# Performance work log

Measured on AMD Instinct MI355X. Metric: run time of the kernel, lower is better.

## Reference

```python
import jax, jax.numpy as jnp
import numpy as np

B, S, H = 2, 2048, 1024
NH, DH = 16, 64  # num heads, head dim

def setup_inputs() -> dict:
    key = jax.random.key(0)
    ks = jax.random.split(key, 4)
    scale = 0.02
    return {
        "hidden_states": jax.random.normal(ks[0], (B, S, H), dtype=jnp.float32),
        "attention_mask": jnp.zeros((B, 1, 1, S), dtype=jnp.float32),  # additive mask
        "Wq": jax.random.normal(ks[1], (H, H), dtype=jnp.float32) * scale,
        "bq": jnp.zeros((H,), dtype=jnp.float32),
        "Wk": jax.random.normal(ks[2], (H, H), dtype=jnp.float32) * scale,
        "bk": jnp.zeros((H,), dtype=jnp.float32),
        "Wv": jax.random.normal(ks[3], (H, H), dtype=jnp.float32) * scale,
        "bv": jnp.zeros((H,), dtype=jnp.float32),
    }

def _split_heads(x):
    # [B,S,H] -> [B,NH,S,DH]
    return x.reshape(B, S, NH, DH).transpose(0, 2, 1, 3)

def reference(hidden_states, attention_mask, Wq, bq, Wk, bk, Wv, bv):
    q = _split_heads(hidden_states @ Wq + bq)
    k = _split_heads(hidden_states @ Wk + bk)
    v = _split_heads(hidden_states @ Wv + bv)
    # scores: [B,NH,S,S]
    scores = jnp.einsum('bhqd,bhkd->bhqk', q, k) / jnp.asarray(np.sqrt(DH), scores_dtype := q.dtype)
    scores = scores + attention_mask  # additive mask broadcast
    probs = jax.nn.softmax(scores, axis=-1)
    out = jnp.einsum('bhqk,bhkd->bhqd', probs, v)  # [B,NH,S,DH]
    out = out.transpose(0, 2, 1, 3).reshape(B, S, H)
    return out
```

## Files before the change

kernel.cpp:

```cpp
#include <hip/hip_runtime.h>
#include <hip/hip_bf16.h>

#define Bn  2
#define Sn  2048
#define Hn  1024
#define NHn 16
#define DHn 64
#define Mn  (Bn * Sn)

typedef __attribute__((ext_vector_type(4)))  float    f32x4;
typedef __attribute__((ext_vector_type(16))) float    f32x16;
typedef __attribute__((ext_vector_type(8)))  _Float16 h8;
typedef __attribute__((ext_vector_type(4)))  _Float16 h4;
typedef __attribute__((ext_vector_type(2)))  __fp16   fp16x2;
typedef __attribute__((ext_vector_type(2)))  unsigned int u32x2;

union H2PK { fp16x2 v; unsigned int u; };
union U4H8 { unsigned int u[4]; h8 v; };

#define MFMA16F(a, b, c) __builtin_amdgcn_mfma_f32_16x16x32_f16(a, b, c, 0, 0, 0)
#define MFMA32F(a, b, c) __builtin_amdgcn_mfma_f32_32x32x16_f16(a, b, c, 0, 0, 0)

#define SCFULL 0.18033688011112042f
#define L2E    1.44269504088896340736f

__device__ __forceinline__ void glds16(const void* g, void* l) {
    __builtin_amdgcn_global_load_lds(
        (const __attribute__((address_space(1))) unsigned int*)g,
        (__attribute__((address_space(3))) unsigned int*)l, 16, 0, 0);
}

__global__ __launch_bounds__(256) void prep(
    const float* __restrict__ X, const float* __restrict__ W0,
    const float* __restrict__ W1, const float* __restrict__ W2,
    _Float16* __restrict__ Xh, _Float16* __restrict__ WT)
{
    const int bid = blockIdx.x;
    const int tid = threadIdx.x;
    __shared__ float Ws[64][65];

    if (bid < 4096) {
        const int i = bid * 256 + tid;
        float4 x = ((const float4*)X)[i];
        h4 o;
        o[0] = (_Float16)x.x; o[1] = (_Float16)x.y;
        o[2] = (_Float16)x.z; o[3] = (_Float16)x.w;
        *(h4*)&Xh[(size_t)i * 4] = o;
        return;
    }

    const int wb = bid - 4096;
    const int which = wb >> 8;
    const int rem = wb & 255;
    const int k0 = ((rem >> 4) & 15) * 64;
    const int n0 = (rem & 15) * 64;
    const float* W = (which == 0) ? W0 : (which == 1 ? W1 : W2);
    _Float16* O = WT + (size_t)which * Hn * Hn;

#pragma unroll
    for (int it = 0; it < 4; ++it) {
        const int idx = tid + 256 * it;
        const int row = idx >> 4, c4 = (idx & 15) * 4;
        float4 w = *(const float4*)&W[(size_t)(k0 + row) * Hn + n0 + c4];
        Ws[row][c4 + 0] = w.x; Ws[row][c4 + 1] = w.y;
        Ws[row][c4 + 2] = w.z; Ws[row][c4 + 3] = w.w;
    }
    __syncthreads();
#pragma unroll
    for (int it = 0; it < 16; ++it) {
        const int e = tid + 256 * it;
        const int k = e & 63, n = e >> 6;
        O[(size_t)(n0 + n) * Hn + k0 + k] = (_Float16)Ws[k][n];
    }
}

__global__ __launch_bounds__(256) void qkv_mfma(
    const _Float16* __restrict__ Xh, const _Float16* __restrict__ WTA,
    const float* __restrict__ b0, const float* __restrict__ b1,
    const float* __restrict__ b2,
    _Float16* __restrict__ Qh, _Float16* __restrict__ Kh,
    _Float16* __restrict__ VTh)
{
    const int which = blockIdx.z;
    const _Float16* WT = WTA + (size_t)which * Hn * Hn;
    const float* bias = (which == 0) ? b0 : (which == 1 ? b1 : b2);
    _Float16* Dst = (which == 0) ? Qh : (which == 1 ? Kh : VTh);

    const int m0 = blockIdx.x * 128;
    const int n0 = blockIdx.y * 128;
    const int tid  = threadIdx.x;
    const int wid  = tid >> 6;
    const int lane = tid & 63;
    const int l16  = lane & 15;
    const int quad = lane >> 4;
    const int wm = wid >> 1, wn = wid & 1;

    __shared__ _Float16 Ah[128 * 64], Bh[128 * 64];

    f32x4 acc[4][4];
#pragma unroll
    for (int i = 0; i < 4; ++i)
#pragma unroll
        for (int j = 0; j < 4; ++j) acc[i][j] = (f32x4){0.f, 0.f, 0.f, 0.f};

    for (int kt = 0; kt < Hn / 64; ++kt) {
        const int k0 = kt * 64;
        __syncthreads();
#pragma unroll
        for (int c = 0; c < 4; ++c) {
            const int idx = (wid * 4 + c) * 64 + lane;
            const int row = idx >> 3;
            const int cg  = (idx & 7) ^ (row & 7);
            glds16(&Xh[(size_t)(m0 + row) * Hn + k0 + cg * 8],
                   &Ah[(wid * 4 + c) * 512]);
            glds16(&WT[(size_t)(n0 + row) * Hn + k0 + cg * 8],
                   &Bh[(wid * 4 + c) * 512]);
        }
        __syncthreads();

#pragma unroll
        for (int kk = 0; kk < 2; ++kk) {
            h8 xa[4], wb[4];
#pragma unroll
            for (int t = 0; t < 4; ++t) {
                const int ar = wm * 64 + t * 16 + l16;
                const int br = wn * 64 + t * 16 + l16;
                xa[t] = *(const h8*)&Ah[ar * 64 + (((kk * 4 + quad) ^ (ar & 7)) * 8)];
                wb[t] = *(const h8*)&Bh[br * 64 + (((kk * 4 + quad) ^ (br & 7)) * 8)];
            }
            if (which < 2) {
#pragma unroll
                for (int i = 0; i < 4; ++i)
#pragma unroll
                    for (int j = 0; j < 4; ++j)
                        acc[i][j] = MFMA16F(xa[i], wb[j], acc[i][j]);
            } else {
#pragma unroll
                for (int i = 0; i < 4; ++i)
#pragma unroll
                    for (int j = 0; j < 4; ++j)
                        acc[i][j] = MFMA16F(wb[i], xa[j], acc[i][j]);
            }
        }
    }

    const float oscale = (which == 0) ? SCFULL : 1.0f;
    if (which < 2) {
#pragma unroll
        for (int j = 0; j < 4; ++j) {
            const int n = n0 + wn * 64 + j * 16 + l16;
            const float bv = bias[n];
            const int hh = n >> 6, dd = n & 63;
#pragma unroll
            for (int i = 0; i < 4; ++i) {
                const int mb = m0 + wm * 64 + i * 16 + quad * 4;
#pragma unroll
                for (int r = 0; r < 4; ++r) {
                    const int m = mb + r;
                    const int b = m >> 11, s = m & (Sn - 1);
                    Dst[(((size_t)b * NHn + hh) * Sn + s) * DHn + dd] =
                        (_Float16)((acc[i][j][r] + bv) * oscale);
                }
            }
        }
    } else {
#pragma unroll
        for (int i = 0; i < 4; ++i) {
#pragma unroll
            for (int r = 0; r < 4; ++r) {
                const int n = n0 + wn * 64 + i * 16 + quad * 4 + r;
                const float bv = bias[n];
                const int hh = n >> 6, dd = n & 63;
#pragma unroll
                for (int j = 0; j < 4; ++j) {
                    const int m = m0 + wm * 64 + j * 16 + l16;
                    const int b = m >> 11, s = m & (Sn - 1);
                    Dst[(((size_t)b * NHn + hh) * DHn + dd) * Sn + s] =
                        (_Float16)(acc[i][j][r] + bv);
                }
            }
        }
    }
}

__global__ __launch_bounds__(256, 2) void attn(
    const _Float16* __restrict__ Qh, const _Float16* __restrict__ Kh,
    const _Float16* __restrict__ VTh, const float* __restrict__ mask,
    float* __restrict__ Out)
{
    const int flat = blockIdx.x + 16 * blockIdx.y + 256 * blockIdx.z;
    const int bh   = ((flat & 7) << 2) | ((flat >> 3) & 3);
    const int qb   = flat >> 5;
    const int b = bh >> 4, h = bh & 15;

    const int tid  = threadIdx.x;
    const int wid  = tid >> 6;
    const int lane = tid & 63;
    const int l32  = lane & 31;
    const int hi   = lane >> 5;

    __shared__ __align__(16) _Float16 Kb[4][4096];
    __shared__ __align__(16) _Float16 Vb[4][4096];
    __shared__ float4 Ml4[Sn / 4];
    const float* Ml = (const float*)Ml4;

    const int q0 = qb * 128 + wid * 32;

    const float4* mg = (const float4*)(mask + (size_t)b * Sn);
    float4 m0v = mg[tid], m1v = mg[tid + 256];

    const size_t qbase = ((size_t)bh * Sn + q0 + l32) * DHn;
    h8 qf[4];
#pragma unroll
    for (int kd = 0; kd < 4; ++kd)
        qf[kd] = *(const h8*)&Qh[qbase + kd * 16 + hi * 8];

    asm volatile("s_waitcnt vmcnt(0)" ::: "memory");

    {
        float4 a0 = {m0v.x * L2E, m0v.y * L2E, m0v.z * L2E, m0v.w * L2E};
        float4 a1 = {m1v.x * L2E, m1v.y * L2E, m1v.z * L2E, m1v.w * L2E};
        Ml4[tid] = a0;
        Ml4[tid + 256] = a1;
    }

    const _Float16* Kg = Kh  + (size_t)bh * Sn * DHn;
    const _Float16* Vg = VTh + (size_t)bh * DHn * Sn;

    auto stage = [&](int kt, int buf) {
        const int koff = kt * 64;
#pragma unroll
        for (int c = 0; c < 2; ++c) {
            const int idx = (wid * 2 + c) * 64 + lane;
            const int row = idx >> 3;
            const int cg  = (idx & 7) ^ (row & 7);
            glds16(&Kg[(size_t)(koff + row) * DHn + cg * 8],
                   &Kb[buf][(wid * 2 + c) * 512]);
            glds16(&Vg[(size_t)row * Sn + koff + cg * 8],
                   &Vb[buf][(wid * 2 + c) * 512]);
        }
    };

    stage(0, 0);
    stage(1, 1);

    f32x16 sA[2], sB[2], o[2], acc_l;
#pragma unroll
    for (int dt = 0; dt < 2; ++dt) o[dt] = (f32x16)(0.f);
    acc_l = (f32x16)(0.f);

    h8 ones;
#pragma unroll
    for (int j = 0; j < 8; ++j) ones[j] = (_Float16)1.0f;

    auto qkt = [&](f32x16 (&s)[2], int buf, int ktile) {
        __builtin_amdgcn_s_setprio(1);
#pragma unroll
        for (int t = 0; t < 2; ++t) {
            f32x16 c;
#pragma unroll
            for (int g = 0; g < 4; ++g) {
                float4 mv = *(const float4*)&Ml[ktile * 64 + t * 32 + hi * 4 + g * 8];
                c[g * 4 + 0] = mv.x; c[g * 4 + 1] = mv.y;
                c[g * 4 + 2] = mv.z; c[g * 4 + 3] = mv.w;
            }
#pragma unroll
            for (int kd = 0; kd < 4; ++kd) {
                const int row = t * 32 + l32;
                h8 kf = *(const h8*)&Kb[buf][row * 64 +
                                             (((kd * 2 + hi) ^ (row & 7)) * 8)];
                c = MFMA32F(kf, qf[kd], c);
            }
            s[t] = c;
        }
        __builtin_amdgcn_s_setprio(0);
    };

    auto sm_pv = [&](f32x16 (&s)[2], int buf) {
        unsigned int pk[2][4][2];
#pragma unroll
        for (int t = 0; t < 2; ++t) {
#pragma unroll
            for (int g = 0; g < 4; ++g) {
                const float p0 = __builtin_amdgcn_exp2f(s[t][g * 4 + 0]);
                const float p1 = __builtin_amdgcn_exp2f(s[t][g * 4 + 1]);
                const float p2 = __builtin_amdgcn_exp2f(s[t][g * 4 + 2]);
                const float p3 = __builtin_amdgcn_exp2f(s[t][g * 4 + 3]);
                H2PK u0, u1;
                u0.v = __builtin_amdgcn_cvt_pkrtz(p0, p1);
                u1.v = __builtin_amdgcn_cvt_pkrtz(p2, p3);
                pk[t][g][0] = u0.u;
                pk[t][g][1] = u1.u;
            }
        }

        __builtin_amdgcn_s_setprio(1);
#pragma unroll
        for (int ks = 0; ks < 4; ++ks) {
            const int t = ks >> 1, ge = (ks & 1) * 2;
            u32x2 rA = __builtin_amdgcn_permlane32_swap(
                pk[t][ge][0], pk[t][ge + 1][0], false, false);
            u32x2 rB = __builtin_amdgcn_permlane32_swap(
                pk[t][ge][1], pk[t][ge + 1][1], false, false);
            U4H8 w;
            w.u[0] = rA[0]; w.u[1] = rB[0]; w.u[2] = rA[1]; w.u[3] = rB[1];
            acc_l = MFMA32F(w.v, ones, acc_l);
#pragma unroll
            for (int dt = 0; dt < 2; ++dt) {
                const int row = dt * 32 + l32;
                h8 vf = *(const h8*)&Vb[buf][row * 64 +
                                             (((ks * 2 + hi) ^ (row & 7)) * 8)];
                o[dt] = MFMA32F(w.v, vf, o[dt]);
            }
        }
        __builtin_amdgcn_s_setprio(0);
    };

    asm volatile("s_waitcnt vmcnt(4) lgkmcnt(0)" ::: "memory");
    __builtin_amdgcn_s_barrier();
    qkt(sA, 0, 0);

    auto iter = [&](int kt, f32x16 (&scur)[2], f32x16 (&snxt)[2]) {
        stage(kt + 2, (kt + 2) & 3);
        asm volatile("s_waitcnt vmcnt(4)" ::: "memory");
        __builtin_amdgcn_s_barrier();
        qkt(snxt, (kt + 1) & 3, kt + 1);
        sm_pv(scur, kt & 3);
    };

    for (int kt = 0; kt < 30; kt += 2) {
        iter(kt,     sA, sB);
        iter(kt + 1, sB, sA);
    }
    asm volatile("s_waitcnt vmcnt(0)" ::: "memory");
    __builtin_amdgcn_s_barrier();
    qkt(sB, 31 & 3, 31);
    sm_pv(sA, 30 & 3);
    sm_pv(sB, 31 & 3);

#pragma unroll
    for (int g2 = 0; g2 < 4; ++g2) {
#pragma unroll
        for (int e = 0; e < 4; ++e) {
            const int r = g2 * 4 + e;
            const int q = q0 + 4 * hi + 8 * g2 + e;
            const size_t ob = ((size_t)b * Sn + q) * Hn + h * DHn;
            const float sc = 1.0f / acc_l[r];
#pragma unroll
            for (int dt = 0; dt < 2; ++dt)
                Out[ob + dt * 32 + l32] = o[dt][r] * sc;
        }
    }
}

extern "C" void kernel_launch(void* const* d_in, const int* in_sizes, int n_in,
                              void* d_out, int out_size, void* d_ws, size_t ws_size,
                              hipStream_t stream) {
    const float* X    = (const float*)d_in[0];
    const float* mask = (const float*)d_in[1];
    const float* Wq   = (const float*)d_in[2];
    const float* bq   = (const float*)d_in[3];
    const float* Wk   = (const float*)d_in[4];
    const float* bk   = (const float*)d_in[5];
    const float* Wv   = (const float*)d_in[6];
    const float* bv   = (const float*)d_in[7];
    float* out = (float*)d_out;

    const size_t NE = (size_t)Mn * Hn;
    _Float16* Xh  = (_Float16*)d_ws;
    _Float16* WT  = Xh + NE;
    _Float16* Qh  = WT + (size_t)3 * Hn * Hn;
    _Float16* Kh  = Qh + NE;
    _Float16* VTh = Kh + NE;

    prep<<<dim3(4096 + 768), dim3(256), 0, stream>>>(X, Wq, Wk, Wv, Xh, WT);

    dim3 g1(Mn / 128, Hn / 128, 3), b1(256);
    qkv_mfma<<<g1, b1, 0, stream>>>(Xh, WT, bq, bk, bv, Qh, Kh, VTh);

    dim3 g2(Sn / 128, NHn, Bn), b2(256);
    attn<<<g2, b2, 0, stream>>>(Qh, Kh, VTh, mask, out);
}
```

Before: 168.2 us.

## Fold additive mask into exp2 weights applied to V and row-sum

The additive mask becomes a per-key multiplicative weight exp2(mask*log2e), computed once in the prep kernel. It is folded into V when V is written out transposed. The attention kernel then stops loading the mask into shared memory and stops initialising score accumulators from it, streaming a small fp16 weight tile alongside K/V for the row-sum MFMA instead. This removes mask reads and per-tile float4 LDS loads from the QK^T loop, at the cost of an extra async load per stage. Because scores no longer include the mask, very negative masks lose the max-stabilisation effect and can underflow in fp16.

After: 171.2 us. Within noise of the previous version (+1.8%).

```diff
diff --git a/kernel.cpp b/kernel.cpp
--- a/kernel.cpp
+++ b/kernel.cpp
@@ -33,7 +33,9 @@
 __global__ __launch_bounds__(256) void prep(
     const float* __restrict__ X, const float* __restrict__ W0,
     const float* __restrict__ W1, const float* __restrict__ W2,
-    _Float16* __restrict__ Xh, _Float16* __restrict__ WT)
+    const float* __restrict__ Msk,
+    _Float16* __restrict__ Xh, _Float16* __restrict__ WT,
+    _Float16* __restrict__ Wm)
 {
     const int bid = blockIdx.x;
     const int tid = threadIdx.x;
@@ -48,6 +50,14 @@
         *(h4*)&Xh[(size_t)i * 4] = o;
         return;
     }
+    if (bid >= 4096 + 768) {
+#pragma unroll
+        for (int it = 0; it < 16; ++it) {
+            const int idx = it * 256 + tid;
+            Wm[idx] = (_Float16)__builtin_amdgcn_exp2f(Msk[idx] * L2E);
+        }
+        return;
+    }
 
     const int wb = bid - 4096;
     const int which = wb >> 8;
@@ -77,7 +87,7 @@
 __global__ __launch_bounds__(256) void qkv_mfma(
     const _Float16* __restrict__ Xh, const _Float16* __restrict__ WTA,
     const float* __restrict__ b0, const float* __restrict__ b1,
-    const float* __restrict__ b2,
+    const float* __restrict__ b2, const _Float16* __restrict__ Wm,
     _Float16* __restrict__ Qh, _Float16* __restrict__ Kh,
     _Float16* __restrict__ VTh)
 {
@@ -164,6 +174,10 @@
             }
         }
     } else {
+        float wvj[4];
+#pragma unroll
+        for (int j = 0; j < 4; ++j)
+            wvj[j] = (float)Wm[m0 + wm * 64 + j * 16 + l16];
 #pragma unroll
         for (int i = 0; i < 4; ++i) {
 #pragma unroll
@@ -176,7 +190,7 @@
                     const int m = m0 + wm * 64 + j * 16 + l16;
                     const int b = m >> 11, s = m & (Sn - 1);
                     Dst[(((size_t)b * NHn + hh) * DHn + dd) * Sn + s] =
-                        (_Float16)(acc[i][j][r] + bv);
+                        (_Float16)((acc[i][j][r] + bv) * wvj[j]);
                 }
             }
         }
@@ -185,7 +199,7 @@
 
 __global__ __launch_bounds__(256, 2) void attn(
     const _Float16* __restrict__ Qh, const _Float16* __restrict__ Kh,
-    const _Float16* __restrict__ VTh, const float* __restrict__ mask,
+    const _Float16* __restrict__ VTh, const _Float16* __restrict__ Wmg,
     float* __restrict__ Out)
 {
     const int flat = blockIdx.x + 16 * blockIdx.y + 256 * blockIdx.z;
@@ -201,13 +215,9 @@
 
     __shared__ __align__(16) _Float16 Kb[4][4096];
     __shared__ __align__(16) _Float16 Vb[4][4096];
-    __shared__ float4 Ml4[Sn / 4];
-    const float* Ml = (const float*)Ml4;
+    __shared__ __align__(16) _Float16 Wb[4][512];
 
     const int q0 = qb * 128 + wid * 32;
-
-    const float4* mg = (const float4*)(mask + (size_t)b * Sn);
-    float4 m0v = mg[tid], m1v = mg[tid + 256];
 
     const size_t qbase = ((size_t)bh * Sn + q0 + l32) * DHn;
     h8 qf[4];
@@ -217,15 +227,9 @@
 
     asm volatile("s_waitcnt vmcnt(0)" ::: "memory");
 
-    {
-        float4 a0 = {m0v.x * L2E, m0v.y * L2E, m0v.z * L2E, m0v.w * L2E};
-        float4 a1 = {m1v.x * L2E, m1v.y * L2E, m1v.z * L2E, m1v.w * L2E};
-        Ml4[tid] = a0;
-        Ml4[tid + 256] = a1;
-    }
-
     const _Float16* Kg = Kh  + (size_t)bh * Sn * DHn;
     const _Float16* Vg = VTh + (size_t)bh * DHn * Sn;
+    const _Float16* Wg = Wmg + (size_t)b * Sn;
 
     auto stage = [&](int kt, int buf) {
         const int koff = kt * 64;
@@ -239,6 +243,7 @@
             glds16(&Vg[(size_t)row * Sn + koff + cg * 8],
                    &Vb[buf][(wid * 2 + c) * 512]);
         }
+        glds16(&Wg[koff + lane * 8], &Wb[buf][0]);
     };
 
     stage(0, 0);
@@ -249,21 +254,11 @@
     for (int dt = 0; dt < 2; ++dt) o[dt] = (f32x16)(0.f);
     acc_l = (f32x16)(0.f);
 
-    h8 ones;
-#pragma unroll
-    for (int j = 0; j < 8; ++j) ones[j] = (_Float16)1.0f;
-
-    auto qkt = [&](f32x16 (&s)[2], int buf, int ktile) {
+    auto qkt = [&](f32x16 (&s)[2], int buf) {
         __builtin_amdgcn_s_setprio(1);
 #pragma unroll
         for (int t = 0; t < 2; ++t) {
-            f32x16 c;
-#pragma unroll
-            for (int g = 0; g < 4; ++g) {
-                float4 mv = *(const float4*)&Ml[ktile * 64 + t * 32 + hi * 4 + g * 8];
-                c[g * 4 + 0] = mv.x; c[g * 4 + 1] = mv.y;
-                c[g * 4 + 2] = mv.z; c[g * 4 + 3] = mv.w;
-            }
+            f32x16 c = (f32x16)(0.f);
 #pragma unroll
             for (int kd = 0; kd < 4; ++kd) {
                 const int row = t * 32 + l32;
@@ -304,7 +299,8 @@
                 pk[t][ge][1], pk[t][ge + 1][1], false, false);
             U4H8 w;
             w.u[0] = rA[0]; w.u[1] = rB[0]; w.u[2] = rA[1]; w.u[3] = rB[1];
-            acc_l = MFMA32F(w.v, ones, acc_l);
+            h8 wv8 = *(const h8*)&Wb[buf][ks * 16 + hi * 8];
+            acc_l = MFMA32F(w.v, wv8, acc_l);
 #pragma unroll
             for (int dt = 0; dt < 2; ++dt) {
                 const int row = dt * 32 + l32;
@@ -316,15 +312,15 @@
         __builtin_amdgcn_s_setprio(0);
     };
 
-    asm volatile("s_waitcnt vmcnt(4) lgkmcnt(0)" ::: "memory");
+    asm volatile("s_waitcnt vmcnt(5)" ::: "memory");
     __builtin_amdgcn_s_barrier();
-    qkt(sA, 0, 0);
+    qkt(sA, 0);
 
     auto iter = [&](int kt, f32x16 (&scur)[2], f32x16 (&snxt)[2]) {
         stage(kt + 2, (kt + 2) & 3);
-        asm volatile("s_waitcnt vmcnt(4)" ::: "memory");
+        asm volatile("s_waitcnt vmcnt(5)" ::: "memory");
         __builtin_amdgcn_s_barrier();
-        qkt(snxt, (kt + 1) & 3, kt + 1);
+        qkt(snxt, (kt + 1) & 3);
         sm_pv(scur, kt & 3);
     };
 
@@ -334,7 +330,7 @@
     }
     asm volatile("s_waitcnt vmcnt(0)" ::: "memory");
     __builtin_amdgcn_s_barrier();
-    qkt(sB, 31 & 3, 31);
+    qkt(sB, 31 & 3);
     sm_pv(sA, 30 & 3);
     sm_pv(sB, 31 & 3);
 
@@ -372,12 +368,14 @@
     _Float16* Qh  = WT + (size_t)3 * Hn * Hn;
     _Float16* Kh  = Qh + NE;
     _Float16* VTh = Kh + NE;
-
-    prep<<<dim3(4096 + 768), dim3(256), 0, stream>>>(X, Wq, Wk, Wv, Xh, WT);
+    _Float16* Wm  = VTh + NE;
+
+    prep<<<dim3(4096 + 768 + 1), dim3(256), 0, stream>>>(
+        X, Wq, Wk, Wv, mask, Xh, WT, Wm);
 
     dim3 g1(Mn / 128, Hn / 128, 3), b1(256);
-    qkv_mfma<<<g1, b1, 0, stream>>>(Xh, WT, bq, bk, bv, Qh, Kh, VTh);
+    qkv_mfma<<<g1, b1, 0, stream>>>(Xh, WT, bq, bk, bv, Wm, Qh, Kh, VTh);
 
     dim3 g2(Sn / 128, NHn, Bn), b2(256);
-    attn<<<g2, b2, 0, stream>>>(Qh, Kh, VTh, mask, out);
-}
+    attn<<<g2, b2, 0, stream>>>(Qh, Kh, VTh, Wm, out);
+}
```
